# Kernel optimization log

Measured on AMD Instinct MI355X. Metric: run time of the kernel, lower is better.

The kernel has to match this reference:

```python
import jax, jax.numpy as jnp
import numpy as np

B, N, NV = 2, 4096, 32768
HID = 128
XD, YD, ZD = 128, 128, 16  # dense occupancy grid dims (original derives from coord maxima)


def setup_inputs() -> dict:
    key = jax.random.key(0)
    ks = jax.random.split(key, 12)
    position = jax.random.normal(ks[0], (B, N, 3), jnp.float32) * 20.0
    scale = jax.random.uniform(ks[1], (B, N, 3), jnp.float32)
    rotation = jax.random.normal(ks[2], (B, N, 4), jnp.float32)
    opacity = jax.random.uniform(ks[3], (B, N, 1), jnp.float32)
    # sparse voxel coords: [batch_idx, x, y, z]
    b_idx = jax.random.randint(ks[4], (NV, 1), 0, B)
    xs = jax.random.randint(ks[5], (NV, 1), 0, XD)
    ys = jax.random.randint(ks[6], (NV, 1), 0, YD)
    zs = jax.random.randint(ks[7], (NV, 1), 0, ZD)
    voxel_coords = jnp.concatenate([b_idx, xs, ys, zs], axis=1).astype(jnp.int32)
    # MLP params: Linear(11,128) -> ReLU -> Linear(128,128)
    W1 = jax.random.normal(ks[8], (11, HID), jnp.float32) * (1.0 / np.sqrt(11))
    b1 = jnp.zeros((HID,), jnp.float32)
    W2 = jax.random.normal(ks[9], (HID, HID), jnp.float32) * (1.0 / np.sqrt(HID))
    b2 = jnp.zeros((HID,), jnp.float32)
    return {"position": position, "scale": scale, "rotation": rotation,
            "opacity": opacity, "W1": W1, "b1": b1, "W2": W2, "b2": b2,
            "voxel_coords": voxel_coords}


def reference(position, scale, rotation, opacity, W1, b1, W2, b2, voxel_coords):
    # concat gaussian attributes -> (B, N, 11)
    x = jnp.concatenate([position, scale, rotation, opacity], axis=-1)
    x = jnp.maximum(x @ W1 + b1, 0.0) @ W2 + b2  # (B, N, HID)

    # anchor grid: linspace(-50,50, N^(1/3))^3 -> (N, 3)
    n_side = int(round(N ** (1.0 / 3.0)))
    anchor_pos = jnp.linspace(-50.0, 50.0, n_side)
    grid = jnp.stack(jnp.meshgrid(anchor_pos, anchor_pos, anchor_pos, indexing="ij"), axis=-1)
    anchor_grid = grid.reshape(-1, 3)  # (N, 3)

    batch_ids = voxel_coords[:, 0]
    xyz = voxel_coords[:, 1:].astype(jnp.float32)  # (NV, 3)

    # Euclidean cdist (NV, N) via ||a||^2 + ||b||^2 - 2ab
    d2 = (jnp.sum(xyz * xyz, axis=1, keepdims=True)
          + jnp.sum(anchor_grid * anchor_grid, axis=1)[None, :]
          - 2.0 * (xyz @ anchor_grid.T))
    dist = jnp.sqrt(jnp.maximum(d2, 0.0))
    weight = jax.nn.softmax(-dist, axis=-1)  # (NV, N)

    fused = jnp.einsum("vn,bnd->bvd", weight, x)  # (B, NV, HID)

    # scatter into dense 5D occupancy grid (vectorized over all batches)
    occ = jnp.zeros((B, HID, XD, YD, ZD), jnp.float32)
    vals = fused[batch_ids, jnp.arange(NV)]  # (NV, HID) per-voxel feature from its own batch
    occ = occ.at[batch_ids, :, voxel_coords[:, 1], voxel_coords[:, 2], voxel_coords[:, 3]].set(vals)
    return occ
```

## Files before the change

kernel.cpp:

```cpp
#include <hip/hip_runtime.h>
#include <hip/hip_bf16.h>

#define B_    2
#define N_    4096
#define NV_   32768
#define HID_  128
#define XD_   128
#define YD_   128
#define ZD_   16
#define PLANE (XD_*YD_*ZD_)
#define LOCS  (B_*PLANE)
#define STEP  (100.0f/15.0f)
#define NT    64
#define VB    64
#define KS    4
#define L2E   1.4426950408889634f

typedef __attribute__((ext_vector_type(8))) short short8;
typedef __attribute__((ext_vector_type(4))) float f32x4;

__device__ __forceinline__ float anchor_coord(int i) {
    return fmaf((float)i, STEP, -50.0f);
}
__device__ __forceinline__ float anchor_s(int i) {
    return fmaf((float)i, STEP * L2E, -50.0f * L2E);
}
__device__ __forceinline__ float fexp2(float x) {
    float r; asm("v_exp_f32 %0, %1" : "=v"(r) : "v"(x)); return r;
}
__device__ __forceinline__ unsigned short f2bf(float x) {
    unsigned u = __float_as_uint(x);
    return (unsigned short)((u + 0x7fffu + ((u >> 16) & 1u)) >> 16);
}

__global__ __launch_bounds__(256) void mlp_kernel(
    const float* __restrict__ pos, const float* __restrict__ scl,
    const float* __restrict__ rot, const float* __restrict__ opa,
    const float* __restrict__ W1,  const float* __restrict__ b1,
    const float* __restrict__ W2,  const float* __restrict__ b2,
    unsigned short* __restrict__ xwT)
{
    int rg = threadIdx.x >> 7;
    int j  = threadIdx.x & 127;
    int r  = blockIdx.x * 2 + rg;
    __shared__ float sin_[2][11];
    __shared__ float h[2][HID_];
    if (j < 11) {
        float val;
        if (j < 3)       val = pos[r*3 + j];
        else if (j < 6)  val = scl[r*3 + (j-3)];
        else if (j < 10) val = rot[r*4 + (j-6)];
        else             val = opa[r];
        sin_[rg][j] = val;
    }
    __syncthreads();
    float a = b1[j];
    #pragma unroll
    for (int i = 0; i < 11; ++i) a = fmaf(sin_[rg][i], W1[i*HID_ + j], a);
    h[rg][j] = fmaxf(a, 0.0f);
    __syncthreads();
    float o = b2[j];
    for (int k = 0; k < HID_; ++k) o = fmaf(h[rg][k], W2[k*HID_ + j], o);
    int b = r >> 12, n = r & 4095;
    xwT[((size_t)(b*HID_ + j))*N_ + n] = f2bf(o);
}

__global__ __launch_bounds__(256) void scatter_kernel(
    const int* __restrict__ vc, int* __restrict__ map,
    int* __restrict__ cnt, int* __restrict__ vlist)
{
    int v = blockIdx.x * 256 + threadIdx.x;
    int4 c = ((const int4*)vc)[v];
    int loc = ((c.x*XD_ + c.y)*YD_ + c.z)*ZD_ + c.w;
    atomicMax(&map[loc], v);
    int lane = threadIdx.x & 63;
    unsigned long long m1 = __ballot(c.x != 0);
    unsigned long long mymask = c.x ? m1 : ~m1;
    int leader = (int)__ffsll(mymask) - 1;
    int total  = __popcll(mymask);
    int rank   = __popcll(mymask & ((1ull << lane) - 1ull));
    int base = 0;
    if (lane == leader) base = atomicAdd(&cnt[c.x], total);
    base = __shfl(base, leader);
    vlist[c.x*NV_ + base + rank] = v;
}

__global__ __launch_bounds__(256) void ml_kernel(
    const int* __restrict__ vc, float2* __restrict__ ml)
{
    int gid = blockIdx.x * 256 + threadIdx.x;
    int v = gid >> 3, sub = gid & 7;
    int4 c = ((const int4*)vc)[v];
    float vx = (float)c.y * L2E, vy = (float)c.z * L2E, vz = (float)c.w * L2E;
    float dz2_[16];
    #pragma unroll 16
    for (int iz = 0; iz < 16; ++iz) { float t = vz - anchor_s(iz); dz2_[iz] = t*t; }

    float m = 1e30f, l = 0.0f;
    #pragma unroll
    for (int i = 0; i < 2; ++i) {
        float dx = vx - anchor_s(sub*2 + i);
        float dx2 = dx*dx;
        for (int iy = 0; iy < 16; ++iy) {
            float dy = vy - anchor_s(iy);
            float bxy = fmaf(dy, dy, dx2);
            #pragma unroll 16
            for (int iz = 0; iz < 16; ++iz) {
                float d = sqrtf(bxy + dz2_[iz]);
                float dm = d - m;
                float e = fexp2(-fabsf(dm));
                bool nm = dm < 0.0f;
                l = nm ? fmaf(l, e, 1.0f) : (l + e);
                m = nm ? d : m;
            }
        }
    }
    #pragma unroll
    for (int off = 1; off < 8; off <<= 1) {
        float m2 = __shfl_xor(m, off);
        float l2 = __shfl_xor(l, off);
        float mn = fminf(m, m2);
        l = l * fexp2(mn - m) + l2 * fexp2(mn - m2);
        m = mn;
    }
    if (sub == 0) ml[v] = make_float2(m, 1.0f / l);
}

__global__ __launch_bounds__(256) void fuse_kernel(
    const unsigned short* __restrict__ xwT, const float2* __restrict__ ml,
    const int* __restrict__ vc,   const int* __restrict__ vlist,
    const int* __restrict__ cnt,  float* __restrict__ fused)
{
    int bid = blockIdx.x;
    int ks_ = bid & (KS-1);
    int rest = bid >> 2;
    int seg = rest >> 9;
    int bi  = rest & 511;
    int count = cnt[seg];
    int vbase = bi * VB;
    if (vbase >= count) return;
    int nv = min(VB, count - vbase);
    int k0 = ks_ * (N_/KS);

    __shared__ uint4 sXT[128*8];
    __shared__ uint4 sP [64*8];
    __shared__ float svx[VB], svy[VB], svz[VB], sdm[VB], sil[VB];
    __shared__ int   svid[VB];

    int tid = threadIdx.x;
    if (tid < VB) {
        int vid = -1; float fx=0, fy=0, fz=0, dm=0, il=0;
        if (tid < nv) {
            vid = vlist[seg*NV_ + vbase + tid];
            int4 c = ((const int4*)vc)[vid];
            fx = (float)c.y * L2E; fy = (float)c.z * L2E; fz = (float)c.w * L2E;
            float2 t = ml[vid]; dm = t.x; il = t.y;
        }
        svid[tid]=vid; svx[tid]=fx; svy[tid]=fy; svz[tid]=fz; sdm[tid]=dm; sil[tid]=il;
    }
    __syncthreads();

    int pv = tid & 63, png = tid >> 6;
    float pvx = svx[pv], pvy = svy[pv], pvz = svz[pv];
    float pml = sdm[pv];
    float dz2_[16];
    #pragma unroll 16
    for (int iz = 0; iz < 16; ++iz) { float t = pvz - anchor_s(iz); dz2_[iz] = t*t; }

    int wv = tid >> 6, L = tid & 63;
    int wr = wv >> 1, wc = wv & 1;
    int r  = L & 15,  g  = L >> 4;
    f32x4 acc[2][4];
    #pragma unroll
    for (int i = 0; i < 2; ++i)
        #pragma unroll
        for (int jj = 0; jj < 4; ++jj) acc[i][jj] = (f32x4){0.f,0.f,0.f,0.f};

    int sd = tid >> 1, ss = tid & 1;
    const uint4* xg = (const uint4*)xwT + ((size_t)(seg*128 + sd) * N_ >> 3);

    for (int t = 0; t < (N_/KS)/NT; ++t) {
        int n0 = k0 + t * NT;
        __syncthreads();
        {
            const uint4* src = xg + (n0 >> 3) + ss*4;
            int dbase = sd * 8;
            #pragma unroll
            for (int i = 0; i < 4; ++i) {
                int blk = ss*4 + i;
                sXT[dbase + (blk ^ (sd & 7))] = src[i];
            }
        }
        {
            int nc = n0 + png*16;
            int idx = nc >> 4;
            float ax = anchor_s(idx >> 4);
            float ay = anchor_s(idx & 15);
            float dxv = pvx - ax, dyv = pvy - ay;
            float bxy = fmaf(dxv, dxv, dyv*dyv);
            unsigned u[8];
            #pragma unroll
            for (int jj = 0; jj < 8; ++jj) {
                float d0 = sqrtf(bxy + dz2_[2*jj]);
                float d1 = sqrtf(bxy + dz2_[2*jj+1]);
                float p0 = fexp2(pml - d0);
                float p1 = fexp2(pml - d1);
                asm("v_cvt_pk_bf16_f32 %0, %1, %2" : "=v"(u[jj]) : "v"(p0), "v"(p1));
            }
            int pb = pv * 8;
            sP[pb + ((png*2    ) ^ (pv & 7))] = make_uint4(u[0],u[1],u[2],u[3]);
            sP[pb + ((png*2 + 1) ^ (pv & 7))] = make_uint4(u[4],u[5],u[6],u[7]);
        }
        __syncthreads();
        #pragma unroll
        for (int kss = 0; kss < 2; ++kss) {
            int blk = kss*4 + g;
            int va0 = wr*32 + r;
            int va1 = va0 + 16;
            short8 a0 = *(const short8*)&sP[va0*8 + (blk ^ (va0 & 7))];
            short8 a1 = *(const short8*)&sP[va1*8 + (blk ^ (va1 & 7))];
            #pragma unroll
            for (int df = 0; df < 4; ++df) {
                int dr = wc*64 + df*16 + r;
                short8 bb = *(const short8*)&sXT[dr*8 + (blk ^ (dr & 7))];
                acc[0][df] = __builtin_amdgcn_mfma_f32_16x16x32_bf16(a0, bb, acc[0][df], 0, 0, 0);
                acc[1][df] = __builtin_amdgcn_mfma_f32_16x16x32_bf16(a1, bb, acc[1][df], 0, 0, 0);
            }
        }
    }

    #pragma unroll
    for (int vi = 0; vi < 2; ++vi)
        #pragma unroll
        for (int df = 0; df < 4; ++df)
            #pragma unroll
            for (int q = 0; q < 4; ++q) {
                int vloc = wr*32 + vi*16 + g*4 + q;
                int dcol = wc*64 + df*16 + r;
                if (vloc < nv) {
                    atomicAdd(&fused[(size_t)svid[vloc]*HID_ + dcol],
                              acc[vi][df][q] * sil[vloc]);
                }
            }
}

__global__ __launch_bounds__(256) void out_kernel(
    const int* __restrict__ map, const float* __restrict__ fused,
    float* __restrict__ out)
{
    int q = blockIdx.x * 256 + threadIdx.x;
    int loc0 = q << 2;
    int b   = loc0 >> 18;
    int rem = loc0 & (PLANE - 1);
    int4 vv = ((const int4*)map)[q];
    const float4* r0 = (const float4*)(fused + (size_t)(vv.x < 0 ? 0 : vv.x) * HID_);
    const float4* r1 = (const float4*)(fused + (size_t)(vv.y < 0 ? 0 : vv.y) * HID_);
    const float4* r2 = (const float4*)(fused + (size_t)(vv.z < 0 ? 0 : vv.z) * HID_);
    const float4* r3 = (const float4*)(fused + (size_t)(vv.w < 0 ? 0 : vv.w) * HID_);
    size_t obase = ((size_t)b * HID_) * PLANE + rem;
    const float4 z4 = make_float4(0.f, 0.f, 0.f, 0.f);
    #pragma unroll 4
    for (int chb = 0; chb < 32; ++chb) {
        float4 a = (vv.x >= 0) ? r0[chb] : z4;
        float4 c = (vv.y >= 0) ? r1[chb] : z4;
        float4 d = (vv.z >= 0) ? r2[chb] : z4;
        float4 e = (vv.w >= 0) ? r3[chb] : z4;
        *(float4*)&out[obase + (size_t)(chb*4 + 0) * PLANE] = make_float4(a.x, c.x, d.x, e.x);
        *(float4*)&out[obase + (size_t)(chb*4 + 1) * PLANE] = make_float4(a.y, c.y, d.y, e.y);
        *(float4*)&out[obase + (size_t)(chb*4 + 2) * PLANE] = make_float4(a.z, c.z, d.z, e.z);
        *(float4*)&out[obase + (size_t)(chb*4 + 3) * PLANE] = make_float4(a.w, c.w, d.w, e.w);
    }
}

extern "C" void kernel_launch(void* const* d_in, const int* in_sizes, int n_in,
                              void* d_out, int out_size, void* d_ws, size_t ws_size,
                              hipStream_t stream) {
    const float* pos = (const float*)d_in[0];
    const float* scl = (const float*)d_in[1];
    const float* rot = (const float*)d_in[2];
    const float* opa = (const float*)d_in[3];
    const float* W1  = (const float*)d_in[4];
    const float* b1  = (const float*)d_in[5];
    const float* W2  = (const float*)d_in[6];
    const float* b2  = (const float*)d_in[7];
    const int*   vc  = (const int*)d_in[8];
    float* out = (float*)d_out;

    char* ws = (char*)d_ws;
    unsigned short* xwT = (unsigned short*)(ws);
    float2* ml    = (float2*)(ws + (2u<<20));
    float*  fused = (float*) (ws + (4u<<20));
    int*    map   = (int*)   (ws + (20u<<20));
    int*    vlist = (int*)   (ws + (22u<<20));
    int*    cnt   = (int*)   (ws + (23u<<20));

    hipMemsetAsync(map, 0xFF, LOCS*sizeof(int), stream);
    hipMemsetAsync(cnt, 0, 2*sizeof(int), stream);
    hipMemsetAsync(fused, 0, (size_t)NV_*HID_*sizeof(float), stream);

    mlp_kernel<<<(B_*N_)/2, 256, 0, stream>>>(pos, scl, rot, opa, W1, b1, W2, b2, xwT);
    scatter_kernel<<<NV_/256, 256, 0, stream>>>(vc, map, cnt, vlist);
    ml_kernel<<<(NV_*8)/256, 256, 0, stream>>>(vc, ml);
    fuse_kernel<<<2*512*KS, 256, 0, stream>>>(xwT, ml, vc, vlist, cnt, fused);
    out_kernel<<<LOCS/(256*4), 256, 0, stream>>>(map, fused, out);
}
```

Baseline: 283.2 us.

## Replace split-K atomicAdd accumulation with per-split partial buffers and a reduce kernel

The fuse kernel now writes each K-split's partial result with plain stores into its own slice of a new partials buffer, instead of atomically adding into one fused buffer. A new reduce kernel sums the four partials and applies the softmax normalisation (1/l) per voxel. This removes the global float atomics and the memset of the fused buffer. In exchange it adds a kernel launch and roughly 64 MB of extra partial-buffer writes and reads, and it moves the workspace layout to make room for that buffer.

```diff
diff --git a/kernel.cpp b/kernel.cpp
--- a/kernel.cpp
+++ b/kernel.cpp
@@ -129,7 +129,7 @@
 __global__ __launch_bounds__(256) void fuse_kernel(
     const unsigned short* __restrict__ xwT, const float2* __restrict__ ml,
     const int* __restrict__ vc,   const int* __restrict__ vlist,
-    const int* __restrict__ cnt,  float* __restrict__ fused)
+    const int* __restrict__ cnt,  float* __restrict__ fused_p)
 {
     int bid = blockIdx.x;
     int ks_ = bid & (KS-1);
@@ -144,19 +144,19 @@
 
     __shared__ uint4 sXT[128*8];
     __shared__ uint4 sP [64*8];
-    __shared__ float svx[VB], svy[VB], svz[VB], sdm[VB], sil[VB];
+    __shared__ float svx[VB], svy[VB], svz[VB], sdm[VB];
     __shared__ int   svid[VB];
 
     int tid = threadIdx.x;
     if (tid < VB) {
-        int vid = -1; float fx=0, fy=0, fz=0, dm=0, il=0;
+        int vid = -1; float fx=0, fy=0, fz=0, dm=0;
         if (tid < nv) {
             vid = vlist[seg*NV_ + vbase + tid];
             int4 c = ((const int4*)vc)[vid];
             fx = (float)c.y * L2E; fy = (float)c.z * L2E; fz = (float)c.w * L2E;
-            float2 t = ml[vid]; dm = t.x; il = t.y;
-        }
-        svid[tid]=vid; svx[tid]=fx; svy[tid]=fy; svz[tid]=fz; sdm[tid]=dm; sil[tid]=il;
+            dm = ml[vid].x;
+        }
+        svid[tid]=vid; svx[tid]=fx; svy[tid]=fy; svz[tid]=fz; sdm[tid]=dm;
     }
     __syncthreads();
 
@@ -229,6 +229,7 @@
         }
     }
 
+    float* fp = fused_p + (size_t)ks_ * NV_ * HID_;
     #pragma unroll
     for (int vi = 0; vi < 2; ++vi)
         #pragma unroll
@@ -238,10 +239,27 @@
                 int vloc = wr*32 + vi*16 + g*4 + q;
                 int dcol = wc*64 + df*16 + r;
                 if (vloc < nv) {
-                    atomicAdd(&fused[(size_t)svid[vloc]*HID_ + dcol],
-                              acc[vi][df][q] * sil[vloc]);
+                    fp[(size_t)svid[vloc]*HID_ + dcol] = acc[vi][df][q];
                 }
             }
+}
+
+__global__ __launch_bounds__(256) void reduce_kernel(
+    const float* __restrict__ fused_p, const float2* __restrict__ ml,
+    float* __restrict__ fused)
+{
+    int idx = blockIdx.x * 256 + threadIdx.x;
+    int v = idx >> 5;
+    float il = ml[v].y;
+    const size_t stride = (size_t)NV_ * HID_ / 4;
+    const float4* p = (const float4*)fused_p + idx;
+    float4 a = p[0], b = p[stride], c = p[2*stride], d = p[3*stride];
+    float4 o;
+    o.x = (a.x + b.x + c.x + d.x) * il;
+    o.y = (a.y + b.y + c.y + d.y) * il;
+    o.z = (a.z + b.z + c.z + d.z) * il;
+    o.w = (a.w + b.w + c.w + d.w) * il;
+    ((float4*)fused)[idx] = o;
 }
 
 __global__ __launch_bounds__(256) void out_kernel(
@@ -288,19 +306,20 @@
 
     char* ws = (char*)d_ws;
     unsigned short* xwT = (unsigned short*)(ws);
-    float2* ml    = (float2*)(ws + (2u<<20));
-    float*  fused = (float*) (ws + (4u<<20));
-    int*    map   = (int*)   (ws + (20u<<20));
-    int*    vlist = (int*)   (ws + (22u<<20));
-    int*    cnt   = (int*)   (ws + (23u<<20));
+    float2* ml      = (float2*)(ws + (2u<<20));
+    float*  fused   = (float*) (ws + (4u<<20));
+    float*  fused_p = (float*) (ws + (20u<<20));
+    int*    map     = (int*)   (ws + (84u<<20));
+    int*    vlist   = (int*)   (ws + (86u<<20));
+    int*    cnt     = (int*)   (ws + (87u<<20));
 
     hipMemsetAsync(map, 0xFF, LOCS*sizeof(int), stream);
     hipMemsetAsync(cnt, 0, 2*sizeof(int), stream);
-    hipMemsetAsync(fused, 0, (size_t)NV_*HID_*sizeof(float), stream);
 
     mlp_kernel<<<(B_*N_)/2, 256, 0, stream>>>(pos, scl, rot, opa, W1, b1, W2, b2, xwT);
     scatter_kernel<<<NV_/256, 256, 0, stream>>>(vc, map, cnt, vlist);
     ml_kernel<<<(NV_*8)/256, 256, 0, stream>>>(vc, ml);
-    fuse_kernel<<<2*512*KS, 256, 0, stream>>>(xwT, ml, vc, vlist, cnt, fused);
+    fuse_kernel<<<2*512*KS, 256, 0, stream>>>(xwT, ml, vc, vlist, cnt, fused_p);
+    reduce_kernel<<<(NV_*HID_/4)/256, 256, 0, stream>>>(fused_p, ml, fused);
     out_kernel<<<LOCS/(256*4), 256, 0, stream>>>(map, fused, out);
 }
```

New measurement: 295.3 us. 1.04x slower.

## Restructure fuse kernel to 32x32 MFMA with register P tiles and per-split partial buffers

Applied to the files above, without the earlier changes.

The fuse kernel now handles 128 voxels per block, using 32x32x16 bf16 MFMAs. The softmax probability A-operand is built directly in registers instead of being staged through LDS. The X tile is loaded with direct global-to-LDS loads. The atomicAdd accumulation over K-splits is replaced by plain stores into four per-split partial buffers, which the output kernel sums and scales by 1/l. This drops the memset of fused and the atomic traffic, at the cost of extra workspace and four times more reads in the output kernel. It also assumes each segment's count fits within 160 blocks of 128 voxels.

```diff
diff --git a/kernel.cpp b/kernel.cpp
--- a/kernel.cpp
+++ b/kernel.cpp
@@ -11,17 +11,13 @@
 #define PLANE (XD_*YD_*ZD_)
 #define LOCS  (B_*PLANE)
 #define STEP  (100.0f/15.0f)
-#define NT    64
-#define VB    64
 #define KS    4
+#define VBL   160
 #define L2E   1.4426950408889634f
 
-typedef __attribute__((ext_vector_type(8))) short short8;
-typedef __attribute__((ext_vector_type(4))) float f32x4;
-
-__device__ __forceinline__ float anchor_coord(int i) {
-    return fmaf((float)i, STEP, -50.0f);
-}
+typedef __attribute__((ext_vector_type(8)))  short short8;
+typedef __attribute__((ext_vector_type(16))) float f32x16;
+
 __device__ __forceinline__ float anchor_s(int i) {
     return fmaf((float)i, STEP * L2E, -50.0f * L2E);
 }
@@ -31,6 +27,11 @@
 __device__ __forceinline__ unsigned short f2bf(float x) {
     unsigned u = __float_as_uint(x);
     return (unsigned short)((u + 0x7fffu + ((u >> 16) & 1u)) >> 16);
+}
+__device__ __forceinline__ void gload16(const void* g, void* l) {
+    __builtin_amdgcn_global_load_lds(
+        (const __attribute__((address_space(1))) unsigned int*)g,
+        (__attribute__((address_space(3))) unsigned int*)l, 16, 0, 0);
 }
 
 __global__ __launch_bounds__(256) void mlp_kernel(
@@ -129,146 +130,150 @@
 __global__ __launch_bounds__(256) void fuse_kernel(
     const unsigned short* __restrict__ xwT, const float2* __restrict__ ml,
     const int* __restrict__ vc,   const int* __restrict__ vlist,
-    const int* __restrict__ cnt,  float* __restrict__ fused)
-{
-    int bid = blockIdx.x;
-    int ks_ = bid & (KS-1);
+    const int* __restrict__ cnt,  float* __restrict__ fused_p)
+{
+    int bid  = blockIdx.x;
+    int ks_  = bid & (KS-1);
     int rest = bid >> 2;
-    int seg = rest >> 9;
-    int bi  = rest & 511;
+    int seg  = (rest >= VBL) ? 1 : 0;
+    int bi   = rest - seg*VBL;
     int count = cnt[seg];
-    int vbase = bi * VB;
+    int vbase = bi * 128;
     if (vbase >= count) return;
-    int nv = min(VB, count - vbase);
+    int nv = min(128, count - vbase);
     int k0 = ks_ * (N_/KS);
 
-    __shared__ uint4 sXT[128*8];
-    __shared__ uint4 sP [64*8];
-    __shared__ float svx[VB], svy[VB], svz[VB], sdm[VB], sil[VB];
-    __shared__ int   svid[VB];
+    __shared__ __align__(16) unsigned char sXT[16384];
+    __shared__ int svid[128];
 
     int tid = threadIdx.x;
-    if (tid < VB) {
-        int vid = -1; float fx=0, fy=0, fz=0, dm=0, il=0;
-        if (tid < nv) {
-            vid = vlist[seg*NV_ + vbase + tid];
-            int4 c = ((const int4*)vc)[vid];
-            fx = (float)c.y * L2E; fy = (float)c.z * L2E; fz = (float)c.w * L2E;
-            float2 t = ml[vid]; dm = t.x; il = t.y;
-        }
-        svid[tid]=vid; svx[tid]=fx; svy[tid]=fy; svz[tid]=fz; sdm[tid]=dm; sil[tid]=il;
-    }
-    __syncthreads();
-
-    int pv = tid & 63, png = tid >> 6;
-    float pvx = svx[pv], pvy = svy[pv], pvz = svz[pv];
-    float pml = sdm[pv];
+    int w  = tid >> 6, l = tid & 63;
+    int h  = l >> 5;
+    int cl = l & 31;
+
+    if (tid < 128) svid[tid] = (tid < nv) ? vlist[seg*NV_ + vbase + tid] : -1;
+
+    int vloc = w*32 + cl;
+    float pml = -1e30f, pvx = 0.f, pvy = 0.f;
     float dz2_[16];
     #pragma unroll 16
-    for (int iz = 0; iz < 16; ++iz) { float t = pvz - anchor_s(iz); dz2_[iz] = t*t; }
-
-    int wv = tid >> 6, L = tid & 63;
-    int wr = wv >> 1, wc = wv & 1;
-    int r  = L & 15,  g  = L >> 4;
-    f32x4 acc[2][4];
-    #pragma unroll
-    for (int i = 0; i < 2; ++i)
-        #pragma unroll
-        for (int jj = 0; jj < 4; ++jj) acc[i][jj] = (f32x4){0.f,0.f,0.f,0.f};
-
-    int sd = tid >> 1, ss = tid & 1;
-    const uint4* xg = (const uint4*)xwT + ((size_t)(seg*128 + sd) * N_ >> 3);
-
-    for (int t = 0; t < (N_/KS)/NT; ++t) {
-        int n0 = k0 + t * NT;
+    for (int iz = 0; iz < 16; ++iz) dz2_[iz] = 0.f;
+    if (vloc < nv) {
+        int vid = vlist[seg*NV_ + vbase + vloc];
+        int4 c = ((const int4*)vc)[vid];
+        pvx = (float)c.y * L2E; pvy = (float)c.z * L2E;
+        float pvz = (float)c.w * L2E;
+        pml = ml[vid].x;
+        #pragma unroll 16
+        for (int iz = 0; iz < 16; ++iz) { float t = pvz - anchor_s(iz); dz2_[iz] = t*t; }
+    }
+
+    int d0s  = w*32 + (l >> 3);
+    int blkX = (l & 7) ^ ((l >> 3) & 7);
+    const unsigned short* sb = xwT + (size_t)(seg*128 + d0s)*N_ + blkX*8 + k0;
+    char* ldsb = (char*)sXT + (size_t)(w*4)*1024;
+
+    f32x16 acc[4];
+    #pragma unroll
+    for (int i = 0; i < 4; ++i) acc[i] = (f32x16)(0.f);
+
+    for (int t = 0; t < (N_/KS)/64; ++t) {
         __syncthreads();
-        {
-            const uint4* src = xg + (n0 >> 3) + ss*4;
-            int dbase = sd * 8;
+        #pragma unroll
+        for (int i = 0; i < 4; ++i)
+            gload16(sb + (size_t)i*8*N_ + t*64, ldsb + i*1024);
+
+        unsigned pk_[4][4];
+        int nb = k0 + t*64;
+        #pragma unroll
+        for (int kss = 0; kss < 4; ++kss) {
+            int kg = nb + kss*16;
+            float ax = anchor_s(kg >> 8);
+            float ay = anchor_s((kg >> 4) & 15);
+            float dx = pvx - ax, dy = pvy - ay;
+            float bxy = fmaf(dx, dx, dy*dy);
             #pragma unroll
-            for (int i = 0; i < 4; ++i) {
-                int blk = ss*4 + i;
-                sXT[dbase + (blk ^ (sd & 7))] = src[i];
+            for (int jj = 0; jj < 4; ++jj) {
+                float dA = sqrtf(bxy + dz2_[h*8 + 2*jj]);
+                float dB = sqrtf(bxy + dz2_[h*8 + 2*jj + 1]);
+                float p0 = fexp2(pml - dA);
+                float p1 = fexp2(pml - dB);
+                asm("v_cvt_pk_bf16_f32 %0, %1, %2" : "=v"(pk_[kss][jj]) : "v"(p0), "v"(p1));
             }
         }
-        {
-            int nc = n0 + png*16;
-            int idx = nc >> 4;
-            float ax = anchor_s(idx >> 4);
-            float ay = anchor_s(idx & 15);
-            float dxv = pvx - ax, dyv = pvy - ay;
-            float bxy = fmaf(dxv, dxv, dyv*dyv);
-            unsigned u[8];
-            #pragma unroll
-            for (int jj = 0; jj < 8; ++jj) {
-                float d0 = sqrtf(bxy + dz2_[2*jj]);
-                float d1 = sqrtf(bxy + dz2_[2*jj+1]);
-                float p0 = fexp2(pml - d0);
-                float p1 = fexp2(pml - d1);
-                asm("v_cvt_pk_bf16_f32 %0, %1, %2" : "=v"(u[jj]) : "v"(p0), "v"(p1));
-            }
-            int pb = pv * 8;
-            sP[pb + ((png*2    ) ^ (pv & 7))] = make_uint4(u[0],u[1],u[2],u[3]);
-            sP[pb + ((png*2 + 1) ^ (pv & 7))] = make_uint4(u[4],u[5],u[6],u[7]);
-        }
         __syncthreads();
-        #pragma unroll
-        for (int kss = 0; kss < 2; ++kss) {
-            int blk = kss*4 + g;
-            int va0 = wr*32 + r;
-            int va1 = va0 + 16;
-            short8 a0 = *(const short8*)&sP[va0*8 + (blk ^ (va0 & 7))];
-            short8 a1 = *(const short8*)&sP[va1*8 + (blk ^ (va1 & 7))];
+
+        #pragma unroll
+        for (int kss = 0; kss < 4; ++kss) {
+            union { uint4 q; short8 s; } u8;
+            u8.q = make_uint4(pk_[kss][0], pk_[kss][1], pk_[kss][2], pk_[kss][3]);
+            short8 af = u8.s;
             #pragma unroll
             for (int df = 0; df < 4; ++df) {
-                int dr = wc*64 + df*16 + r;
-                short8 bb = *(const short8*)&sXT[dr*8 + (blk ^ (dr & 7))];
-                acc[0][df] = __builtin_amdgcn_mfma_f32_16x16x32_bf16(a0, bb, acc[0][df], 0, 0, 0);
-                acc[1][df] = __builtin_amdgcn_mfma_f32_16x16x32_bf16(a1, bb, acc[1][df], 0, 0, 0);
+                int row = df*32 + cl;
+                int blk = (kss*2 + h) ^ (row & 7);
+                short8 bf = *(const short8*)&sXT[row*128 + blk*16];
+                acc[df] = __builtin_amdgcn_mfma_f32_32x32x16_bf16(af, bf, acc[df], 0, 0, 0);
             }
         }
     }
 
-    #pragma unroll
-    for (int vi = 0; vi < 2; ++vi)
-        #pragma unroll
-        for (int df = 0; df < 4; ++df)
-            #pragma unroll
-            for (int q = 0; q < 4; ++q) {
-                int vloc = wr*32 + vi*16 + g*4 + q;
-                int dcol = wc*64 + df*16 + r;
-                if (vloc < nv) {
-                    atomicAdd(&fused[(size_t)svid[vloc]*HID_ + dcol],
-                              acc[vi][df][q] * sil[vloc]);
-                }
-            }
+    float* fp = fused_p + (size_t)ks_ * NV_ * HID_;
+    #pragma unroll
+    for (int df = 0; df < 4; ++df) {
+        int dcol = df*32 + cl;
+        #pragma unroll
+        for (int reg = 0; reg < 16; ++reg) {
+            int vrow = w*32 + (reg & 3) + 8*(reg >> 2) + 4*h;
+            int sv = svid[vrow];
+            if (sv >= 0) fp[(size_t)sv*HID_ + dcol] = acc[df][reg];
+        }
+    }
 }
 
 __global__ __launch_bounds__(256) void out_kernel(
-    const int* __restrict__ map, const float* __restrict__ fused,
-    float* __restrict__ out)
+    const int* __restrict__ map, const float* __restrict__ fused_p,
+    const float2* __restrict__ ml, float* __restrict__ out)
 {
     int q = blockIdx.x * 256 + threadIdx.x;
     int loc0 = q << 2;
     int b   = loc0 >> 18;
     int rem = loc0 & (PLANE - 1);
     int4 vv = ((const int4*)map)[q];
-    const float4* r0 = (const float4*)(fused + (size_t)(vv.x < 0 ? 0 : vv.x) * HID_);
-    const float4* r1 = (const float4*)(fused + (size_t)(vv.y < 0 ? 0 : vv.y) * HID_);
-    const float4* r2 = (const float4*)(fused + (size_t)(vv.z < 0 ? 0 : vv.z) * HID_);
-    const float4* r3 = (const float4*)(fused + (size_t)(vv.w < 0 ? 0 : vv.w) * HID_);
     size_t obase = ((size_t)b * HID_) * PLANE + rem;
-    const float4 z4 = make_float4(0.f, 0.f, 0.f, 0.f);
-    #pragma unroll 4
+    const size_t S4 = (size_t)NV_ * HID_ / 4;
+    const float4* P = (const float4*)fused_p;
+
+    int   va[4] = {vv.x, vv.y, vv.z, vv.w};
+    float il[4];
+    const float4* rp[4];
+    #pragma unroll
+    for (int k = 0; k < 4; ++k) {
+        il[k] = (va[k] >= 0) ? ml[va[k]].y : 0.0f;
+        rp[k] = P + (size_t)(va[k] >= 0 ? va[k] : 0) * 32;
+    }
+
     for (int chb = 0; chb < 32; ++chb) {
-        float4 a = (vv.x >= 0) ? r0[chb] : z4;
-        float4 c = (vv.y >= 0) ? r1[chb] : z4;
-        float4 d = (vv.z >= 0) ? r2[chb] : z4;
-        float4 e = (vv.w >= 0) ? r3[chb] : z4;
-        *(float4*)&out[obase + (size_t)(chb*4 + 0) * PLANE] = make_float4(a.x, c.x, d.x, e.x);
-        *(float4*)&out[obase + (size_t)(chb*4 + 1) * PLANE] = make_float4(a.y, c.y, d.y, e.y);
-        *(float4*)&out[obase + (size_t)(chb*4 + 2) * PLANE] = make_float4(a.z, c.z, d.z, e.z);
-        *(float4*)&out[obase + (size_t)(chb*4 + 3) * PLANE] = make_float4(a.w, c.w, d.w, e.w);
+        float4 vals[4];
+        #pragma unroll
+        for (int k = 0; k < 4; ++k) {
+            float4 s = make_float4(0.f, 0.f, 0.f, 0.f);
+            if (va[k] >= 0) {
+                float4 a = rp[k][chb];
+                float4 bq = rp[k][chb + S4];
+                float4 cq = rp[k][chb + 2*S4];
+                float4 dq = rp[k][chb + 3*S4];
+                s.x = (a.x + bq.x + cq.x + dq.x) * il[k];
+                s.y = (a.y + bq.y + cq.y + dq.y) * il[k];
+                s.z = (a.z + bq.z + cq.z + dq.z) * il[k];
+                s.w = (a.w + bq.w + cq.w + dq.w) * il[k];
+            }
+            vals[k] = s;
+        }
+        *(float4*)&out[obase + (size_t)(chb*4 + 0) * PLANE] = make_float4(vals[0].x, vals[1].x, vals[2].x, vals[3].x);
+        *(float4*)&out[obase + (size_t)(chb*4 + 1) * PLANE] = make_float4(vals[0].y, vals[1].y, vals[2].y, vals[3].y);
+        *(float4*)&out[obase + (size_t)(chb*4 + 2) * PLANE] = make_float4(vals[0].z, vals[1].z, vals[2].z, vals[3].z);
+        *(float4*)&out[obase + (size_t)(chb*4 + 3) * PLANE] = make_float4(vals[0].w, vals[1].w, vals[2].w, vals[3].w);
     }
 }
 
@@ -288,19 +293,18 @@
 
     char* ws = (char*)d_ws;
     unsigned short* xwT = (unsigned short*)(ws);
-    float2* ml    = (float2*)(ws + (2u<<20));
-    float*  fused = (float*) (ws + (4u<<20));
-    int*    map   = (int*)   (ws + (20u<<20));
-    int*    vlist = (int*)   (ws + (22u<<20));
-    int*    cnt   = (int*)   (ws + (23u<<20));
+    float2* ml      = (float2*)(ws + (2u<<20));
+    float*  fused_p = (float*) (ws + (4u<<20));
+    int*    map     = (int*)   (ws + (72u<<20));
+    int*    vlist   = (int*)   (ws + (74u<<20));
+    int*    cnt     = (int*)   (ws + (75u<<20));
 
     hipMemsetAsync(map, 0xFF, LOCS*sizeof(int), stream);
     hipMemsetAsync(cnt, 0, 2*sizeof(int), stream);
-    hipMemsetAsync(fused, 0, (size_t)NV_*HID_*sizeof(float), stream);
 
     mlp_kernel<<<(B_*N_)/2, 256, 0, stream>>>(pos, scl, rot, opa, W1, b1, W2, b2, xwT);
     scatter_kernel<<<NV_/256, 256, 0, stream>>>(vc, map, cnt, vlist);
     ml_kernel<<<(NV_*8)/256, 256, 0, stream>>>(vc, ml);
-    fuse_kernel<<<2*512*KS, 256, 0, stream>>>(xwT, ml, vc, vlist, cnt, fused);
-    out_kernel<<<LOCS/(256*4), 256, 0, stream>>>(map, fused, out);
-}
+    fuse_kernel<<<2*VBL*KS, 256, 0, stream>>>(xwT, ml, vc, vlist, cnt, fused_p);
+    out_kernel<<<LOCS/(256*4), 256, 0, stream>>>(map, fused_p, ml, out);
+}
```

New measurement: 312.0 us. 10.2% more time.
